# Kernel tuning notes

Measured on AMD Instinct MI355X. Metric: run time of the kernel, lower is better.

Reference implementation:

```python
import jax, jax.numpy as jnp
import numpy as np

B, S, D, H = 1, 2048, 1280, 16
HD = D // H  # 80


def setup_inputs() -> dict:
    key = jax.random.key(0)
    ks = jax.random.split(key, 6)
    return {
        "hidden_states": jax.random.normal(ks[0], (B, S, D), dtype=jnp.float32),
        "rotary_pos_emb": jax.random.normal(ks[1], (S, HD // 2), dtype=jnp.float32),
        "qkv_w": jax.random.normal(ks[2], (3 * D, D), dtype=jnp.float32) * 0.02,
        "qkv_b": jax.random.normal(ks[3], (3 * D,), dtype=jnp.float32) * 0.02,
        "proj_w": jax.random.normal(ks[4], (D, D), dtype=jnp.float32) * 0.02,
        "proj_b": jax.random.normal(ks[5], (D,), dtype=jnp.float32) * 0.02,
    }


def reference(hidden_states, rotary_pos_emb, qkv_w, qkv_b, proj_w, proj_b):
    b, s, d = hidden_states.shape
    h = H
    hd = d // h
    scaling = hd ** -0.5

    # fused QKV projection: [b, s, 3*d]
    qkv = hidden_states @ qkv_w.T + qkv_b
    qkv = qkv.reshape(b, s, 3, h, hd)
    q, k, v = qkv[:, :, 0], qkv[:, :, 1], qkv[:, :, 2]  # each [b, s, h, hd]

    # rotary embedding: cos/sin [s, hd//2] -> [1, s, 1, hd]
    cos = jnp.cos(rotary_pos_emb)
    sin = jnp.sin(rotary_pos_emb)
    cos = jnp.concatenate([cos, cos], axis=-1)[None, :, None, :]
    sin = jnp.concatenate([sin, sin], axis=-1)[None, :, None, :]

    def apply_rope(x):
        x1, x2 = x[..., : hd // 2], x[..., hd // 2:]
        return x * cos + jnp.concatenate([-x2, x1], axis=-1) * sin

    q = apply_rope(q)
    k = apply_rope(k)

    # [b, h, s, hd]
    q = q.transpose(0, 2, 1, 3)
    k = k.transpose(0, 2, 1, 3)
    v = v.transpose(0, 2, 1, 3)

    # naive full attention matrix [b, h, s, s]
    attn = jnp.einsum("bhqd,bhkd->bhqk", q, k) * scaling
    attn = jax.nn.softmax(attn, axis=-1)
    out = jnp.einsum("bhqk,bhkd->bhqd", attn, v)
    out = out.transpose(0, 2, 1, 3).reshape(b, s, d)
    return out @ proj_w.T + proj_b
```

## Files before the change

kernel.cpp:

```cpp
#include <hip/hip_runtime.h>
#include <math.h>

#define SS 2048
#define DD 1280
#define HH 16
#define HDD 80
#define ND3 3840

typedef __attribute__((ext_vector_type(8))) short short8;
typedef __attribute__((ext_vector_type(4))) short s16x4;
typedef __attribute__((ext_vector_type(4))) float f32x4;
typedef __attribute__((ext_vector_type(8))) _Float16 h16x8;
typedef __attribute__((ext_vector_type(4))) _Float16 h16x4;

__device__ inline short f2bf(float f) {
    union { float f; unsigned u; } x; x.f = f;
    unsigned r = x.u + 0x7FFF + ((x.u >> 16) & 1);
    return (short)(r >> 16);
}

__global__ __launch_bounds__(256) void split_f16(
    const float* __restrict__ a, _Float16* __restrict__ ah, int nbA,
    const float* __restrict__ b, _Float16* __restrict__ bh, int nbB,
    const float* __restrict__ c, _Float16* __restrict__ ch)
{
    const float* x; _Float16* h;
    int blk = blockIdx.x;
    if (blk < nbA)            { x = a; h = ah; }
    else if (blk < nbA + nbB) { blk -= nbA; x = b; h = bh; }
    else                      { blk -= nbA + nbB; x = c; h = ch; }
    int i = (blk * 256 + threadIdx.x) * 4;
    float4 v = *(const float4*)(x + i);
    h16x4 hv;
    hv[0] = (_Float16)v.x; hv[1] = (_Float16)v.y;
    hv[2] = (_Float16)v.z; hv[3] = (_Float16)v.w;
    *(h16x4*)(h + i) = hv;
}

#define LDSA(m, kg) ((m) * 32 + (((kg) ^ (((m) >> 1) & 3)) << 3))

template <int BMT, int BNT>
__global__ __launch_bounds__(256) void gemm_f16(
    const _Float16* __restrict__ Ah, const _Float16* __restrict__ Bh,
    const float* __restrict__ bias, float* __restrict__ C,
    int M, int N, int K)
{
    constexpr int IT = BMT / 32;
    constexpr int JT = BNT / 32;
    constexpr int AU = BMT / 64;
    constexpr int BU = BNT / 64;
    __shared__ _Float16 AhS[BMT * 32];
    __shared__ _Float16 BhS[BNT * 32];

    const int tid = threadIdx.x;
    const int w = tid >> 6;
    const int lane = tid & 63;
    const int l15 = lane & 15;
    const int quad = lane >> 4;
    const int wm = w >> 1, wn = w & 1;
    const int bm = blockIdx.y * BMT;
    const int bn = blockIdx.x * BNT;

    f32x4 acc[IT][JT];
    #pragma unroll
    for (int i = 0; i < IT; ++i)
        #pragma unroll
        for (int j = 0; j < JT; ++j)
            acc[i][j] = (f32x4){0.f, 0.f, 0.f, 0.f};

    h16x8 rah[AU], rbh[BU];
    auto loadg = [&](int k0) {
        #pragma unroll
        for (int u = 0; u < AU; ++u) {
            int c = tid + u * 256, m = c >> 2, kg = c & 3;
            rah[u] = *(const h16x8*)(Ah + (size_t)(bm + m) * K + k0 + kg * 8);
        }
        #pragma unroll
        for (int u = 0; u < BU; ++u) {
            int c = tid + u * 256, m = c >> 2, kg = c & 3;
            rbh[u] = *(const h16x8*)(Bh + (size_t)(bn + m) * K + k0 + kg * 8);
        }
    };

    loadg(0);
    for (int k0 = 0; k0 < K; k0 += 32) {
        __syncthreads();
        #pragma unroll
        for (int u = 0; u < AU; ++u) {
            int c = tid + u * 256, m = c >> 2, kg = c & 3;
            *(h16x8*)&AhS[LDSA(m, kg)] = rah[u];
        }
        #pragma unroll
        for (int u = 0; u < BU; ++u) {
            int c = tid + u * 256, m = c >> 2, kg = c & 3;
            *(h16x8*)&BhS[LDSA(m, kg)] = rbh[u];
        }
        __syncthreads();
        if (k0 + 32 < K) loadg(k0 + 32);

        h16x8 af[IT], bf[JT];
        #pragma unroll
        for (int i = 0; i < IT; ++i) {
            int m = wm * (BMT / 2) + i * 16 + l15;
            af[i] = *(h16x8*)&AhS[LDSA(m, quad)];
        }
        #pragma unroll
        for (int j = 0; j < JT; ++j) {
            int n = wn * (BNT / 2) + j * 16 + l15;
            bf[j] = *(h16x8*)&BhS[LDSA(n, quad)];
        }
        #pragma unroll
        for (int i = 0; i < IT; ++i)
            #pragma unroll
            for (int j = 0; j < JT; ++j)
                acc[i][j] = __builtin_amdgcn_mfma_f32_16x16x32_f16(af[i], bf[j], acc[i][j], 0, 0, 0);
    }

    #pragma unroll
    for (int j = 0; j < JT; ++j) {
        int col = bn + wn * (BNT / 2) + j * 16 + l15;
        float bb = bias[col];
        #pragma unroll
        for (int i = 0; i < IT; ++i)
            #pragma unroll
            for (int r = 0; r < 4; ++r) {
                int row = bm + wm * (BMT / 2) + i * 16 + quad * 4 + r;
                C[(size_t)row * N + col] = acc[i][j][r] + bb;
            }
    }
}

__global__ __launch_bounds__(256) void gemm_proj_merge(
    const _Float16* __restrict__ o_part, const float* __restrict__ l_part,
    const _Float16* __restrict__ Bh,
    const float* __restrict__ bias, float* __restrict__ C,
    int M, int N, int K)
{
    constexpr int BMT = 64, BNT = 128;
    constexpr int JT = BNT / 32;
    constexpr int BU = BNT / 64;
    __shared__ _Float16 AhS[BMT * 32];
    __shared__ _Float16 BhS[BNT * 32];
    __shared__ float linvS[HH * 64];

    const int tid = threadIdx.x;
    const int w = tid >> 6;
    const int lane = tid & 63;
    const int l15 = lane & 15;
    const int quad = lane >> 4;
    const int wm = w >> 1, wn = w & 1;
    const int bm = blockIdx.y * BMT;
    const int bn = blockIdx.x * BNT;

    for (int i = tid; i < HH * 64; i += 256) {
        int h = i >> 6, r = i & 63;
        float l0 = l_part[(size_t)h * SS + bm + r];
        float l1 = l_part[(size_t)(HH + h) * SS + bm + r];
        linvS[i] = 1.f / (l0 + l1);
    }

    f32x4 acc[2][JT];
    #pragma unroll
    for (int i = 0; i < 2; ++i)
        #pragma unroll
        for (int j = 0; j < JT; ++j)
            acc[i][j] = (f32x4){0.f, 0.f, 0.f, 0.f};

    h16x8 ra0, ra1, rbh[BU];
    auto loadg = [&](int k0) {
        {
            int m = tid >> 2, kg = tid & 3;
            size_t off = (size_t)(bm + m) * K + k0 + kg * 8;
            ra0 = *(const h16x8*)(o_part + off);
            ra1 = *(const h16x8*)(o_part + (size_t)SS * DD + off);
        }
        #pragma unroll
        for (int u = 0; u < BU; ++u) {
            int c = tid + u * 256, m = c >> 2, kg = c & 3;
            rbh[u] = *(const h16x8*)(Bh + (size_t)(bn + m) * K + k0 + kg * 8);
        }
    };

    loadg(0);
    for (int k0 = 0; k0 < K; k0 += 32) {
        __syncthreads();
        {
            int m = tid >> 2, kg = tid & 3;
            int koff = k0 + kg * 8;
            int h = koff / HDD;
            float inv = linvS[h * 64 + m];
            h16x8 f;
            #pragma unroll
            for (int e = 0; e < 8; ++e)
                f[e] = (_Float16)(((float)ra0[e] + (float)ra1[e]) * inv);
            *(h16x8*)&AhS[LDSA(m, kg)] = f;
        }
        #pragma unroll
        for (int u = 0; u < BU; ++u) {
            int c = tid + u * 256, m = c >> 2, kg = c & 3;
            *(h16x8*)&BhS[LDSA(m, kg)] = rbh[u];
        }
        __syncthreads();
        if (k0 + 32 < K) loadg(k0 + 32);

        h16x8 af[2], bf[JT];
        #pragma unroll
        for (int i = 0; i < 2; ++i) {
            int m = wm * 32 + i * 16 + l15;
            af[i] = *(h16x8*)&AhS[LDSA(m, quad)];
        }
        #pragma unroll
        for (int j = 0; j < JT; ++j) {
            int n = wn * 64 + j * 16 + l15;
            bf[j] = *(h16x8*)&BhS[LDSA(n, quad)];
        }
        #pragma unroll
        for (int i = 0; i < 2; ++i)
            #pragma unroll
            for (int j = 0; j < JT; ++j)
                acc[i][j] = __builtin_amdgcn_mfma_f32_16x16x32_f16(af[i], bf[j], acc[i][j], 0, 0, 0);
    }

    #pragma unroll
    for (int j = 0; j < JT; ++j) {
        int col = bn + wn * 64 + j * 16 + l15;
        float bb = bias[col];
        #pragma unroll
        for (int i = 0; i < 2; ++i)
            #pragma unroll
            for (int r = 0; r < 4; ++r) {
                int row = bm + wm * 32 + i * 16 + quad * 4 + r;
                C[(size_t)row * N + col] = acc[i][j][r] + bb;
            }
    }
}

__global__ __launch_bounds__(256) void rope_scatter_bf16(
    const float* __restrict__ qkv, const float* __restrict__ rpe,
    short* __restrict__ q, short* __restrict__ k, short* __restrict__ v)
{
    __shared__ __align__(16) float cs[40], sn[40];
    const int s = blockIdx.x;
    if (threadIdx.x < 40)
        __sincosf(rpe[s * 40 + threadIdx.x], &sn[threadIdx.x], &cs[threadIdx.x]);
    __syncthreads();
    const float scale = 0.11180339887498949f;
    const float* src = qkv + (size_t)s * ND3;
    for (int t = threadIdx.x; t < ND3 / 4; t += 256) {
        int j4 = t * 4;
        int p = j4 / DD;
        int rem = j4 - p * DD;
        int hh = rem / HDD;
        int d = rem - hh * HDD;
        float4 x = *(const float4*)(src + j4);
        float vv[4];
        if (p == 2) {
            vv[0] = x.x; vv[1] = x.y; vv[2] = x.z; vv[3] = x.w;
        } else {
            bool lo = d < 40;
            int dm = lo ? d : d - 40;
            float4 oth = *(const float4*)(src + p * DD + hh * HDD + (lo ? d + 40 : d - 40));
            float4 c4 = *(const float4*)&cs[dm];
            float4 s4 = *(const float4*)&sn[dm];
            float sg = lo ? -1.f : 1.f;
            vv[0] = x.x * c4.x + sg * oth.x * s4.x;
            vv[1] = x.y * c4.y + sg * oth.y * s4.y;
            vv[2] = x.z * c4.z + sg * oth.z * s4.z;
            vv[3] = x.w * c4.w + sg * oth.w * s4.w;
            if (p == 0) { vv[0] *= scale; vv[1] *= scale; vv[2] *= scale; vv[3] *= scale; }
        }
        short* dst = (p == 0) ? q : (p == 1) ? k : v;
        s16x4 o4;
        o4[0] = f2bf(vv[0]); o4[1] = f2bf(vv[1]);
        o4[2] = f2bf(vv[2]); o4[3] = f2bf(vv[3]);
        *(s16x4*)(dst + ((size_t)hh * SS + s) * HDD + d) = o4;
    }
}

__global__ __launch_bounds__(256) void attn_mfma(
    const short* __restrict__ q, const short* __restrict__ k,
    const short* __restrict__ v, _Float16* __restrict__ o_part,
    float* __restrict__ l_part)
{
    __shared__ short Ks[64][104];
    __shared__ short Vts[80 * 64];
    __shared__ short Ps[4][32][72];

    const int h = blockIdx.y;
    const int q0 = blockIdx.x << 7;
    const int z = blockIdx.z;
    const int tid = threadIdx.x;
    const int w = tid >> 6;
    const int lane = tid & 63;
    const int l15 = lane & 15;
    const int quad = lane >> 4;

    const short* qbase = q + (size_t)h * SS * HDD;
    const short* kbase = k + (size_t)h * SS * HDD;
    const short* vbase = v + (size_t)h * SS * HDD;

    short8 qf[2][3];
    #pragma unroll
    for (int i = 0; i < 2; ++i) {
        const int row = q0 + w * 32 + i * 16 + l15;
        #pragma unroll
        for (int kk = 0; kk < 3; ++kk) {
            int c0 = kk * 32 + quad * 8;
            qf[i][kk] = (c0 < HDD) ? *(const short8*)(qbase + (size_t)row * HDD + c0)
                                   : (short8)0;
        }
    }

    if (tid < 128) {
        int r = tid >> 1, c = 80 + (tid & 1) * 8;
        *(short8*)&Ks[r][c] = (short8)0;
    }

    float lsum[2][4] = {{0.f}};
    f32x4 o[2][5];
    #pragma unroll
    for (int i = 0; i < 2; ++i)
        #pragma unroll
        for (int n = 0; n < 5; ++n) o[i][n] = (f32x4){0.f, 0.f, 0.f, 0.f};

    const int kt0 = z << 10;
    for (int kt = kt0; kt < kt0 + 1024; kt += 64) {
        __syncthreads();
        #pragma unroll
        for (int u = 0; u < 3; ++u) {
            int i = tid + u * 256;
            if (i < 640) {
                int r = i / 10, c = (i - r * 10) * 8;
                *(short8*)&Ks[r][c] = *(const short8*)(kbase + (size_t)(kt + r) * HDD + c);
            }
        }
        #pragma unroll
        for (int u = 0; u < 2; ++u) {
            int task = tid + u * 256;
            if (task < 320) {
                int r4 = (task & 15) << 2;
                int d4 = (task >> 4) << 2;
                s16x4 a0 = *(const s16x4*)(vbase + (size_t)(kt + r4 + 0) * HDD + d4);
                s16x4 a1 = *(const s16x4*)(vbase + (size_t)(kt + r4 + 1) * HDD + d4);
                s16x4 a2 = *(const s16x4*)(vbase + (size_t)(kt + r4 + 2) * HDD + d4);
                s16x4 a3 = *(const s16x4*)(vbase + (size_t)(kt + r4 + 3) * HDD + d4);
                #pragma unroll
                for (int j = 0; j < 4; ++j) {
                    s16x4 w4 = {a0[j], a1[j], a2[j], a3[j]};
                    int d = d4 + j;
                    int sw = (r4 >> 3) ^ (d & 7);
                    *(s16x4*)&Vts[d * 64 + sw * 8 + (r4 & 7)] = w4;
                }
            }
        }
        __syncthreads();

        f32x4 s_[2][4];
        #pragma unroll
        for (int nt = 0; nt < 4; ++nt) {
            short8 bf0 = *(short8*)&Ks[nt * 16 + l15][quad * 8];
            short8 bf1 = *(short8*)&Ks[nt * 16 + l15][32 + quad * 8];
            short8 bf2 = *(short8*)&Ks[nt * 16 + l15][64 + quad * 8];
            #pragma unroll
            for (int i = 0; i < 2; ++i) {
                f32x4 acc = (f32x4){0.f, 0.f, 0.f, 0.f};
                acc = __builtin_amdgcn_mfma_f32_16x16x32_bf16(qf[i][0], bf0, acc, 0, 0, 0);
                acc = __builtin_amdgcn_mfma_f32_16x16x32_bf16(qf[i][1], bf1, acc, 0, 0, 0);
                acc = __builtin_amdgcn_mfma_f32_16x16x32_bf16(qf[i][2], bf2, acc, 0, 0, 0);
                s_[i][nt] = acc;
            }
        }

        #pragma unroll
        for (int i = 0; i < 2; ++i)
            #pragma unroll
            for (int nt = 0; nt < 4; ++nt)
                #pragma unroll
                for (int r = 0; r < 4; ++r) {
                    float p = __expf(s_[i][nt][r] - 8.f);
                    lsum[i][r] += p;
                    Ps[w][i * 16 + quad * 4 + r][nt * 16 + l15] = f2bf(p);
                }

        short8 pf[2][2];
        #pragma unroll
        for (int i = 0; i < 2; ++i)
            #pragma unroll
            for (int kk = 0; kk < 2; ++kk)
                pf[i][kk] = *(short8*)&Ps[w][i * 16 + l15][kk * 32 + quad * 8];
        #pragma unroll
        for (int n = 0; n < 5; ++n) {
            #pragma unroll
            for (int kk = 0; kk < 2; ++kk) {
                int d = n * 16 + l15;
                int sw = (kk * 4 + quad) ^ (l15 & 7);
                short8 vf = *(short8*)&Vts[d * 64 + sw * 8];
                #pragma unroll
                for (int i = 0; i < 2; ++i)
                    o[i][n] = __builtin_amdgcn_mfma_f32_16x16x32_bf16(pf[i][kk], vf, o[i][n], 0, 0, 0);
            }
        }
    }

    _Float16* ob = o_part + (size_t)z * SS * DD;
    #pragma unroll
    for (int i = 0; i < 2; ++i) {
        #pragma unroll
        for (int r = 0; r < 4; ++r) {
            float rs = lsum[i][r];
            #pragma unroll
            for (int off = 1; off < 16; off <<= 1)
                rs += __shfl_xor(rs, off, 64);
            lsum[i][r] = rs;
        }
        #pragma unroll
        for (int n = 0; n < 5; ++n)
            #pragma unroll
            for (int r = 0; r < 4; ++r) {
                int row = q0 + w * 32 + i * 16 + quad * 4 + r;
                ob[(size_t)row * DD + h * HDD + n * 16 + l15] = (_Float16)o[i][n][r];
            }
        if (l15 == 0)
            #pragma unroll
            for (int r = 0; r < 4; ++r)
                l_part[((size_t)z * HH + h) * SS + q0 + w * 32 + i * 16 + quad * 4 + r] = lsum[i][r];
    }
}

extern "C" void kernel_launch(void* const* d_in, const int* in_sizes, int n_in,
                              void* d_out, int out_size, void* d_ws, size_t ws_size,
                              hipStream_t stream)
{
    const float* hs     = (const float*)d_in[0];
    const float* rpe    = (const float*)d_in[1];
    const float* qkv_w  = (const float*)d_in[2];
    const float* qkv_b  = (const float*)d_in[3];
    const float* proj_w = (const float*)d_in[4];
    const float* proj_b = (const float*)d_in[5];
    float* out = (float*)d_out;

    short* s0 = (short*)d_ws;
    float* qkv_f  = (float*)d_ws;
    _Float16* o_part = (_Float16*)s0;
    float* l_part = (float*)(s0 + 10485760);
    short* s1 = s0 + 15728640;
    _Float16* qkvw_h = (_Float16*)s1;
    short* qb = s1;
    short* kb = s1 + 2621440;
    short* vb = s1 + 5242880;
    short* s2 = s1 + 7864320;
    _Float16* hs_h = (_Float16*)s2;
    short* s3 = s2 + 2621440;
    _Float16* projw_h = (_Float16*)s3;

    const int n_hs = SS * DD;
    const int n_qw = ND3 * DD;
    const int n_pw = DD * DD;

    split_f16<<<n_hs / 1024 + n_qw / 1024 + n_pw / 1024, 256, 0, stream>>>(
        hs, hs_h, n_hs / 1024,
        qkv_w, qkvw_h, n_qw / 1024,
        proj_w, projw_h);
    gemm_f16<128, 128><<<dim3(ND3 / 128, SS / 128), 256, 0, stream>>>(
        hs_h, qkvw_h, qkv_b, qkv_f, SS, ND3, DD);
    rope_scatter_bf16<<<SS, 256, 0, stream>>>(qkv_f, rpe, qb, kb, vb);
    attn_mfma<<<dim3(SS / 128, HH, 2), 256, 0, stream>>>(qb, kb, vb, o_part, l_part);
    gemm_proj_merge<<<dim3(DD / 128, SS / 64), 256, 0, stream>>>(
        o_part, l_part, projw_h, proj_b, out, SS, DD, DD);
}
```

Measured before the change: 211.3 us.

## Raise attention KV split to four partitions and swizzle P tile in LDS

The attention kernel now splits the key range into four chunks instead of two, launching twice as many blocks so more CUs stay busy. The projection GEMM's merge step is generalized to sum four partial outputs and four partial row sums. Separately, the per-wave P tile in LDS drops its row padding and uses an XOR swizzle to avoid bank conflicts on the write and read paths. In exchange, the merge GEMM reads twice as much partial-output data, and the o_part/l_part workspace must be large enough for four partitions.

```diff
diff --git a/kernel.cpp b/kernel.cpp
--- a/kernel.cpp
+++ b/kernel.cpp
@@ -6,6 +6,7 @@
 #define HH 16
 #define HDD 80
 #define ND3 3840
+#define ZZ 4
 
 typedef __attribute__((ext_vector_type(8))) short short8;
 typedef __attribute__((ext_vector_type(4))) short s16x4;
@@ -154,9 +155,11 @@
 
     for (int i = tid; i < HH * 64; i += 256) {
         int h = i >> 6, r = i & 63;
-        float l0 = l_part[(size_t)h * SS + bm + r];
-        float l1 = l_part[(size_t)(HH + h) * SS + bm + r];
-        linvS[i] = 1.f / (l0 + l1);
+        float ls = 0.f;
+        #pragma unroll
+        for (int zi = 0; zi < ZZ; ++zi)
+            ls += l_part[((size_t)zi * HH + h) * SS + bm + r];
+        linvS[i] = 1.f / ls;
     }
 
     f32x4 acc[2][JT];
@@ -166,13 +169,14 @@
         for (int j = 0; j < JT; ++j)
             acc[i][j] = (f32x4){0.f, 0.f, 0.f, 0.f};
 
-    h16x8 ra0, ra1, rbh[BU];
+    h16x8 ra[ZZ], rbh[BU];
     auto loadg = [&](int k0) {
         {
             int m = tid >> 2, kg = tid & 3;
             size_t off = (size_t)(bm + m) * K + k0 + kg * 8;
-            ra0 = *(const h16x8*)(o_part + off);
-            ra1 = *(const h16x8*)(o_part + (size_t)SS * DD + off);
+            #pragma unroll
+            for (int zi = 0; zi < ZZ; ++zi)
+                ra[zi] = *(const h16x8*)(o_part + (size_t)zi * SS * DD + off);
         }
         #pragma unroll
         for (int u = 0; u < BU; ++u) {
@@ -191,8 +195,12 @@
             float inv = linvS[h * 64 + m];
             h16x8 f;
             #pragma unroll
-            for (int e = 0; e < 8; ++e)
-                f[e] = (_Float16)(((float)ra0[e] + (float)ra1[e]) * inv);
+            for (int e = 0; e < 8; ++e) {
+                float s = (float)ra[0][e];
+                #pragma unroll
+                for (int zi = 1; zi < ZZ; ++zi) s += (float)ra[zi][e];
+                f[e] = (_Float16)(s * inv);
+            }
             *(h16x8*)&AhS[LDSA(m, kg)] = f;
         }
         #pragma unroll
@@ -284,7 +292,7 @@
 {
     __shared__ short Ks[64][104];
     __shared__ short Vts[80 * 64];
-    __shared__ short Ps[4][32][72];
+    __shared__ short Ps[4][32 * 64];
 
     const int h = blockIdx.y;
     const int q0 = blockIdx.x << 7;
@@ -323,8 +331,8 @@
         #pragma unroll
         for (int n = 0; n < 5; ++n) o[i][n] = (f32x4){0.f, 0.f, 0.f, 0.f};
 
-    const int kt0 = z << 10;
-    for (int kt = kt0; kt < kt0 + 1024; kt += 64) {
+    const int kt0 = z << 9;
+    for (int kt = kt0; kt < kt0 + 512; kt += 64) {
         __syncthreads();
         #pragma unroll
         for (int u = 0; u < 3; ++u) {
@@ -379,15 +387,19 @@
                 for (int r = 0; r < 4; ++r) {
                     float p = __expf(s_[i][nt][r] - 8.f);
                     lsum[i][r] += p;
-                    Ps[w][i * 16 + quad * 4 + r][nt * 16 + l15] = f2bf(p);
+                    int row = i * 16 + quad * 4 + r;
+                    int g = (nt * 2 + (l15 >> 3)) ^ (row & 7);
+                    Ps[w][row * 64 + g * 8 + (l15 & 7)] = f2bf(p);
                 }
 
         short8 pf[2][2];
         #pragma unroll
         for (int i = 0; i < 2; ++i)
             #pragma unroll
-            for (int kk = 0; kk < 2; ++kk)
-                pf[i][kk] = *(short8*)&Ps[w][i * 16 + l15][kk * 32 + quad * 8];
+            for (int kk = 0; kk < 2; ++kk) {
+                int g = (kk * 4 + quad) ^ (l15 & 7);
+                pf[i][kk] = *(short8*)&Ps[w][(i * 16 + l15) * 64 + g * 8];
+            }
         #pragma unroll
         for (int n = 0; n < 5; ++n) {
             #pragma unroll
@@ -464,7 +476,7 @@
     gemm_f16<128, 128><<<dim3(ND3 / 128, SS / 128), 256, 0, stream>>>(
         hs_h, qkvw_h, qkv_b, qkv_f, SS, ND3, DD);
     rope_scatter_bf16<<<SS, 256, 0, stream>>>(qkv_f, rpe, qb, kb, vb);
-    attn_mfma<<<dim3(SS / 128, HH, 2), 256, 0, stream>>>(qb, kb, vb, o_part, l_part);
+    attn_mfma<<<dim3(SS / 128, HH, ZZ), 256, 0, stream>>>(qb, kb, vb, o_part, l_part);
     gemm_proj_merge<<<dim3(DD / 128, SS / 64), 256, 0, stream>>>(
         o_part, l_part, projw_h, proj_b, out, SS, DD, DD);
 }
```

New measurement: 226.1 us. 1.07x slower.
